# Kernel optimization log

Measured on AMD Instinct MI355X. Metric: run time of the kernel, lower is better.

The kernel has to match this reference:

```python
import jax, jax.numpy as jnp
import numpy as np

ALPHA = 0.2  # leaky relu slope
NEG_BIG = -9000000000000000.0


def setup_inputs() -> dict:
    key = jax.random.key(0)
    k1, k2, k3, k4 = jax.random.split(key, 4)
    B, N, Fin, Fout = 8, 2048, 256, 256
    h = jax.random.normal(k1, (B, N, Fin), dtype=jnp.float32)
    adj = jax.random.randint(k2, (B, N, N), 0, 2, dtype=jnp.int32)
    # xavier_uniform with gain=1.414
    gain = 1.414
    limW = gain * np.sqrt(6.0 / (Fin + Fout))
    W = jax.random.uniform(k3, (Fin, Fout), dtype=jnp.float32, minval=-limW, maxval=limW)
    lima = gain * np.sqrt(6.0 / (2 * Fout + 1))
    a = jax.random.uniform(k4, (2 * Fout, 1), dtype=jnp.float32, minval=-lima, maxval=lima)
    return {"h": h, "adj": adj, "W": W, "a": a}


def reference(h, adj, W, a):
    # Wh: [B, N, F]
    Wh = jnp.matmul(h, W)
    Fout = W.shape[1]
    a1 = a[:Fout, 0]   # scores for source node i (repeat_interleave side)
    a2 = a[Fout:, 0]   # scores for target node j (repeat side)
    # e[b,i,j] = leakyrelu(Wh[b,i]@a1 + Wh[b,j]@a2)  -- decomposed, no O(N^2 * 2F) tensor
    s1 = jnp.einsum('bnf,f->bn', Wh, a1)  # [B, N]
    s2 = jnp.einsum('bnf,f->bn', Wh, a2)  # [B, N]
    e = jax.nn.leaky_relu(s1[:, :, None] + s2[:, None, :], negative_slope=ALPHA)
    masked = jnp.where(adj > 0, e, jnp.full_like(e, NEG_BIG))
    attention = jax.nn.softmax(masked, axis=2)  # dropout=0 (eval mode)
    h_prime = jnp.matmul(attention, Wh)  # [B, N, F]
    return jax.nn.elu(h_prime)
```

## Files before the change

### kernel.cpp

```cpp
#include <hip/hip_runtime.h>

typedef __attribute__((ext_vector_type(8))) short bhalf8;
typedef __attribute__((ext_vector_type(4))) float floatx4;

#define ALPHA_LR 0.2f

__device__ __forceinline__ unsigned short f2bf(float f) {
  union { float f; unsigned int u; } v; v.f = f;
  unsigned int r = v.u + 0x7fffu + ((v.u >> 16) & 1u);
  return (unsigned short)(r >> 16);
}
__device__ __forceinline__ float bf2f(unsigned short u) {
  union { unsigned int u; float f; } v; v.u = ((unsigned int)u) << 16;
  return v.f;
}
__device__ __forceinline__ void gld16(const void* g, void* l) {
  __builtin_amdgcn_global_load_lds((const __attribute__((address_space(1))) unsigned int*)g,
                                   (__attribute__((address_space(3))) unsigned int*)l,
                                   16, 0, 0);
}

__global__ void k0w_split(const float* __restrict__ W,
                          unsigned short* __restrict__ WThi,
                          unsigned short* __restrict__ WTlo) {
  __shared__ float s[16][17];
  const int tx = threadIdx.x, ty = threadIdx.y;
  const int n0 = blockIdx.x * 16, k0 = blockIdx.y * 16;
  s[ty][tx] = W[(k0 + ty) * 256 + n0 + tx];
  __syncthreads();
  float v = s[tx][ty];
  const int k = k0 + tx, n = n0 + ty;
  unsigned short hi = f2bf(v);
  unsigned short lo = f2bf(v - bf2f(hi));
  const int idx = (k >> 5) * 8192 + n * 32 + (k & 31);
  WThi[idx] = hi;
  WTlo[idx] = lo;
}

__global__ __launch_bounds__(512, 2) void k1_mfma(const float* __restrict__ h,
                                                  const unsigned short* __restrict__ Bhi_g,
                                                  const unsigned short* __restrict__ Blo_g,
                                                  const float* __restrict__ a_g,
                                                  unsigned short* __restrict__ WhPack,
                                                  float* __restrict__ s1,
                                                  float* __restrict__ s2) {
  __shared__ unsigned short Ah[64 * 264], Al[64 * 264];
  __shared__ unsigned short Bh[2][8192], Bl[2][8192];
  __shared__ float s1red[64], s2red[64];
  const int t = threadIdx.x;
  const long r0 = (long)blockIdx.x * 64;
  const int wave = t >> 6, lane = t & 63;

  if (t < 64) { s1red[t] = 0.f; s2red[t] = 0.f; }

#pragma unroll
  for (int rep = 0; rep < 2; rep++) {
    const int off = wave * 1024 + rep * 512;
    gld16(Bhi_g + off + lane * 8, &Bh[0][off]);
    gld16(Blo_g + off + lane * 8, &Bl[0][off]);
  }

#pragma unroll
  for (int q = 0; q < 8; q++) {
    int idx = q * 512 + t;
    int row = idx >> 6, c4 = idx & 63;
    float4 x = *(const float4*)(h + (r0 + row) * 256 + c4 * 4);
    float xs[4] = {x.x, x.y, x.z, x.w};
    unsigned short hs[4], ls[4];
#pragma unroll
    for (int qq = 0; qq < 4; qq++) {
      hs[qq] = f2bf(xs[qq]);
      ls[qq] = f2bf(xs[qq] - bf2f(hs[qq]));
    }
    *(ushort4*)&Ah[row * 264 + c4 * 4] = (ushort4){hs[0], hs[1], hs[2], hs[3]};
    *(ushort4*)&Al[row * 264 + c4 * 4] = (ushort4){ls[0], ls[1], ls[2], ls[3]};
  }
  __syncthreads();

  const int wm = wave >> 2, wn = wave & 3;
  const int lhi = lane >> 4, llo = lane & 15;

  floatx4 acc[2][4];
#pragma unroll
  for (int mt = 0; mt < 2; mt++)
#pragma unroll
    for (int nt = 0; nt < 4; nt++) acc[mt][nt] = (floatx4){0.f, 0.f, 0.f, 0.f};

  for (int ks = 0; ks < 8; ks++) {
    const int cur = ks & 1, nxt = cur ^ 1, ksn = (ks + 1) & 7;
#pragma unroll
    for (int rep = 0; rep < 2; rep++) {
      const int off = wave * 1024 + rep * 512;
      gld16(Bhi_g + ksn * 8192 + off + lane * 8, &Bh[nxt][off]);
      gld16(Blo_g + ksn * 8192 + off + lane * 8, &Bl[nxt][off]);
    }

    const int k0 = ks * 32;
    bhalf8 ah[2], al[2], bh[4], bl[4];
#pragma unroll
    for (int mt = 0; mt < 2; mt++) {
      int ro = (wm * 32 + mt * 16 + llo) * 264 + k0 + lhi * 8;
      ah[mt] = *(const bhalf8*)&Ah[ro];
      al[mt] = *(const bhalf8*)&Al[ro];
    }
#pragma unroll
    for (int nt = 0; nt < 4; nt++) {
      int ro = (wn * 64 + nt * 16 + llo) * 32 + lhi * 8;
      bh[nt] = *(const bhalf8*)&Bh[cur][ro];
      bl[nt] = *(const bhalf8*)&Bl[cur][ro];
    }
#pragma unroll
    for (int mt = 0; mt < 2; mt++)
#pragma unroll
      for (int nt = 0; nt < 4; nt++) {
        acc[mt][nt] = __builtin_amdgcn_mfma_f32_16x16x32_bf16(ah[mt], bh[nt], acc[mt][nt], 0, 0, 0);
        acc[mt][nt] = __builtin_amdgcn_mfma_f32_16x16x32_bf16(ah[mt], bl[nt], acc[mt][nt], 0, 0, 0);
        acc[mt][nt] = __builtin_amdgcn_mfma_f32_16x16x32_bf16(al[mt], bh[nt], acc[mt][nt], 0, 0, 0);
      }
    __syncthreads();
  }

  float a1v[4], a2v[4];
#pragma unroll
  for (int nt = 0; nt < 4; nt++) {
    int f = wn * 64 + nt * 16 + llo;
    a1v[nt] = a_g[f];
    a2v[nt] = a_g[256 + f];
  }

  const int b = (int)(r0 >> 11);
  const int jt_base = (int)((r0 & 2047) >> 5);

#pragma unroll
  for (int mt = 0; mt < 2; mt++) {
    float p1[4], p2[4];
#pragma unroll
    for (int reg = 0; reg < 4; reg++) {
      p1[reg] = acc[mt][0][reg] * a1v[0] + acc[mt][1][reg] * a1v[1] +
                acc[mt][2][reg] * a1v[2] + acc[mt][3][reg] * a1v[3];
      p2[reg] = acc[mt][0][reg] * a2v[0] + acc[mt][1][reg] * a2v[1] +
                acc[mt][2][reg] * a2v[2] + acc[mt][3][reg] * a2v[3];
    }
#pragma unroll
    for (int off = 1; off < 16; off <<= 1) {
#pragma unroll
      for (int reg = 0; reg < 4; reg++) {
        p1[reg] += __shfl_xor(p1[reg], off);
        p2[reg] += __shfl_xor(p2[reg], off);
      }
    }
    if (llo == 0) {
#pragma unroll
      for (int reg = 0; reg < 4; reg++) {
        int il = wm * 32 + mt * 16 + lhi * 4 + reg;
        atomicAdd(&s1red[il], p1[reg]);
        atomicAdd(&s2red[il], p2[reg]);
      }
    }
#pragma unroll
    for (int nt = 0; nt < 4; nt++) {
      int f = wn * 64 + nt * 16 + llo;
      int jt = jt_base + wm;
      ushort4 pk = (ushort4){f2bf(acc[mt][nt][0]), f2bf(acc[mt][nt][1]),
                             f2bf(acc[mt][nt][2]), f2bf(acc[mt][nt][3])};
      *(ushort4*)&WhPack[((long)((b * 64 + jt) * 256 + f)) * 32 + mt * 16 + lhi * 4] = pk;
    }
  }

  __syncthreads();
  if (t < 64) {
    s1[r0 + t] = s1red[t];
    s2[r0 + t] = s2red[t];
  }
}

__global__ __launch_bounds__(256) void k2_stats(const int* __restrict__ adj,
                                                const float* __restrict__ s1,
                                                const float* __restrict__ s2,
                                                float* __restrict__ Mv,
                                                float* __restrict__ linv,
                                                unsigned int* __restrict__ packed) {
  const int t = threadIdx.x;
  const long r = blockIdx.x;
  const int b = (int)(r >> 11);
  __shared__ float red[4];
  __shared__ int redi[4];
  __shared__ unsigned char bytes[256];

  const int4* arow = (const int4*)(adj + r * 2048);
  int4 a0 = arow[t * 2], a1 = arow[t * 2 + 1];
  unsigned int m8 = (unsigned)(a0.x > 0) | ((unsigned)(a0.y > 0) << 1) |
                    ((unsigned)(a0.z > 0) << 2) | ((unsigned)(a0.w > 0) << 3) |
                    ((unsigned)(a1.x > 0) << 4) | ((unsigned)(a1.y > 0) << 5) |
                    ((unsigned)(a1.z > 0) << 6) | ((unsigned)(a1.w > 0) << 7);

  int cnt = __popc(m8);
  for (int o = 32; o; o >>= 1) cnt += __shfl_xor(cnt, o);
  if ((t & 63) == 0) redi[t >> 6] = cnt;
  __syncthreads();
  int total = redi[0] + redi[1] + redi[2] + redi[3];
  if (total == 0) m8 = 0xFFu;

  const float4* s2p = (const float4*)(s2 + (long)b * 2048);
  float4 v0 = s2p[t * 2], v1 = s2p[t * 2 + 1];
  float sv[8] = {v0.x, v0.y, v0.z, v0.w, v1.x, v1.y, v1.z, v1.w};

  float mx = -INFINITY;
#pragma unroll
  for (int q = 0; q < 8; q++)
    if ((m8 >> q) & 1) mx = fmaxf(mx, sv[q]);
  for (int o = 32; o; o >>= 1) mx = fmaxf(mx, __shfl_xor(mx, o));
  if ((t & 63) == 0) red[t >> 6] = mx;
  __syncthreads();
  mx = fmaxf(fmaxf(red[0], red[1]), fmaxf(red[2], red[3]));

  const float s1i = s1[r];
  const float xm = s1i + mx;
  const float M = fmaxf(xm, ALPHA_LR * xm);

  float lsum = 0.f;
#pragma unroll
  for (int q = 0; q < 8; q++) {
    if ((m8 >> q) & 1) {
      float x = s1i + sv[q];
      float le = fmaxf(x, ALPHA_LR * x);
      lsum += __expf(le - M);
    }
  }
  for (int o = 32; o; o >>= 1) lsum += __shfl_xor(lsum, o);
  __syncthreads();
  if ((t & 63) == 0) red[t >> 6] = lsum;
  __syncthreads();
  lsum = red[0] + red[1] + red[2] + red[3];

  if (t == 0) { Mv[r] = M; linv[r] = 1.f / lsum; }

  bytes[t] = (unsigned char)m8;
  __syncthreads();
  if (t < 64) {
    unsigned int w = (unsigned)bytes[t * 4] | ((unsigned)bytes[t * 4 + 1] << 8) |
                     ((unsigned)bytes[t * 4 + 2] << 16) | ((unsigned)bytes[t * 4 + 3] << 24);
    packed[r * 64 + t] = w;
  }
}

__global__ __launch_bounds__(512, 4) void k3_attn(const unsigned short* __restrict__ WhPack,
                                                  const unsigned int* __restrict__ packed,
                                                  const float* __restrict__ s1,
                                                  const float* __restrict__ s2,
                                                  const float* __restrict__ Mv,
                                                  const float* __restrict__ linv,
                                                  float* __restrict__ out) {
  const int t = threadIdx.x;
  const int it = blockIdx.x;
  const int b = blockIdx.y;
  const int i0 = it * 32;

  __shared__ float s2all[2048];
  __shared__ unsigned int bits[2048];
  __shared__ float s1v[32], Mvv[32], lvv[32];
  __shared__ unsigned short WhT[2][8192];
  __shared__ unsigned short P[2][1280];

  {
    const float4* src = (const float4*)(s2 + (long)b * 2048);
    ((float4*)s2all)[t] = src[t];
  }
  {
    const int4* src = (const int4*)(packed + ((long)b * 2048 + i0) * 64);
    ((int4*)bits)[t] = src[t];
  }
  if (t < 32) {
    long r = (long)b * 2048 + i0 + t;
    s1v[t] = s1[r]; Mvv[t] = Mv[r]; lvv[t] = linv[r];
  }
  __syncthreads();

  const int wave = t >> 6, lane = t & 63;
  const int wm = wave >> 2, wn = wave & 3;
  const int lhi = lane >> 4, llo = lane & 15;
  const int i_p = t >> 4;
  const int jl0 = (t & 15) * 2;

  const unsigned short* tbase = WhPack + ((long)b * 64) * 8192;

#pragma unroll
  for (int rep = 0; rep < 2; rep++) {
    const int off = wave * 1024 + rep * 512;
    gld16(tbase + off + lane * 8, &WhT[0][off]);
  }
  {
    unsigned int w = bits[i_p * 64 + 0];
    float s1i = s1v[i_p], Mi = Mvv[i_p];
    unsigned short pb[2];
#pragma unroll
    for (int q = 0; q < 2; q++) {
      int jl = jl0 + q;
      float x = s1i + s2all[jl];
      float le = fmaxf(x, ALPHA_LR * x);
      float pu = ((w >> jl) & 1u) ? __expf(le - Mi) : 0.f;
      pb[q] = f2bf(pu);
    }
    *(unsigned int*)&P[0][i_p * 40 + jl0] = (unsigned)pb[0] | ((unsigned)pb[1] << 16);
  }
  __syncthreads();

  floatx4 acc[4];
#pragma unroll
  for (int nt = 0; nt < 4; nt++) acc[nt] = (floatx4){0.f, 0.f, 0.f, 0.f};

  for (int jt = 0; jt < 64; jt++) {
    const int cur = jt & 1, nxt = cur ^ 1, jtn = (jt + 1) & 63;

#pragma unroll
    for (int rep = 0; rep < 2; rep++) {
      const int off = wave * 1024 + rep * 512;
      gld16(tbase + jtn * 8192 + off + lane * 8, &WhT[nxt][off]);
    }
    {
      unsigned int w = bits[i_p * 64 + jtn];
      float s1i = s1v[i_p], Mi = Mvv[i_p];
      unsigned short pb[2];
#pragma unroll
      for (int q = 0; q < 2; q++) {
        int jl = jl0 + q;
        float x = s1i + s2all[jtn * 32 + jl];
        float le = fmaxf(x, ALPHA_LR * x);
        float pu = ((w >> jl) & 1u) ? __expf(le - Mi) : 0.f;
        pb[q] = f2bf(pu);
      }
      *(unsigned int*)&P[nxt][i_p * 40 + jl0] = (unsigned)pb[0] | ((unsigned)pb[1] << 16);
    }
    bhalf8 af = *(const bhalf8*)&P[cur][(wm * 16 + llo) * 40 + lhi * 8];
    bhalf8 bf[4];
#pragma unroll
    for (int nt = 0; nt < 4; nt++)
      bf[nt] = *(const bhalf8*)&WhT[cur][(wn * 64 + nt * 16 + llo) * 32 + lhi * 8];
#pragma unroll
    for (int nt = 0; nt < 4; nt++)
      acc[nt] = __builtin_amdgcn_mfma_f32_16x16x32_bf16(af, bf[nt], acc[nt], 0, 0, 0);
    __syncthreads();
  }

#pragma unroll
  for (int nt = 0; nt < 4; nt++) {
#pragma unroll
    for (int reg = 0; reg < 4; reg++) {
      int il = wm * 16 + lhi * 4 + reg;
      int f = wn * 64 + nt * 16 + llo;
      float v = acc[nt][reg] * lvv[il];
      v = v > 0.f ? v : expm1f(v);
      out[((long)(b * 2048 + i0 + il)) * 256 + f] = v;
    }
  }
}

extern "C" void kernel_launch(void* const* d_in, const int* in_sizes, int n_in,
                              void* d_out, int out_size, void* d_ws, size_t ws_size,
                              hipStream_t stream) {
  const float* h = (const float*)d_in[0];
  const int* adj = (const int*)d_in[1];
  const float* W = (const float*)d_in[2];
  const float* a = (const float*)d_in[3];
  float* out = (float*)d_out;

  char* ws = (char*)d_ws;
  unsigned short* WhPack = (unsigned short*)ws;
  unsigned int* packed = (unsigned int*)(ws + 8388608);
  unsigned short* WThi = (unsigned short*)(ws + 12582912);
  unsigned short* WTlo = (unsigned short*)(ws + 12713984);
  float* s1 = (float*)(ws + 12845056);
  float* s2 = (float*)(ws + 12910592);
  float* Mv = (float*)(ws + 12976128);
  float* linv = (float*)(ws + 13041664);

  hipLaunchKernelGGL(k0w_split, dim3(16, 16), dim3(16, 16), 0, stream, W, WThi, WTlo);
  hipLaunchKernelGGL(k1_mfma, dim3(256), dim3(512), 0, stream, h, WThi, WTlo, a,
                     WhPack, s1, s2);
  hipLaunchKernelGGL(k2_stats, dim3(16384), dim3(256), 0, stream, adj, s1, s2, Mv, linv, packed);
  hipLaunchKernelGGL(k3_attn, dim3(64, 8), dim3(512), 0, stream, WhPack, packed, s1, s2, Mv, linv, out);
}
```

Baseline: 265.4 us.

## Retile attention kernel: 128-row by 64-feature blocks, P in registers, B from global

The attention-times-Wh kernel now tiles 128 rows by 64 output features per 256-thread block, replacing 32 rows by all 256 features. Each wave computes its P fragments directly in registers from the mask bits and s1/s2, so the shared-memory P buffer and the per-step __syncthreads go away. Wh fragments are loaded straight from global into registers with a two-deep software prefetch, where before they were staged into LDS via global_load_lds. The grid grows to 512 blocks, and the exp work is now repeated across the four feature-chunk blocks, which adds redundant transcendental computation.

```diff
diff --git a/kernel.cpp b/kernel.cpp
--- a/kernel.cpp
+++ b/kernel.cpp
@@ -244,113 +244,121 @@
   }
 }
 
-__global__ __launch_bounds__(512, 4) void k3_attn(const unsigned short* __restrict__ WhPack,
+__global__ __launch_bounds__(256, 3) void k3_attn(const unsigned short* __restrict__ WhPack,
                                                   const unsigned int* __restrict__ packed,
-                                                  const float* __restrict__ s1,
-                                                  const float* __restrict__ s2,
-                                                  const float* __restrict__ Mv,
-                                                  const float* __restrict__ linv,
+                                                  const float* __restrict__ s1g,
+                                                  const float* __restrict__ s2g,
+                                                  const float* __restrict__ Mg,
+                                                  const float* __restrict__ lg,
                                                   float* __restrict__ out) {
   const int t = threadIdx.x;
-  const int it = blockIdx.x;
-  const int b = blockIdx.y;
-  const int i0 = it * 32;
+  const int fc = blockIdx.x;
+  const int ry = blockIdx.y;
+  const int b = blockIdx.z;
+  const int rowbase = ry * 128;
 
   __shared__ float s2all[2048];
-  __shared__ unsigned int bits[2048];
-  __shared__ float s1v[32], Mvv[32], lvv[32];
-  __shared__ unsigned short WhT[2][8192];
-  __shared__ unsigned short P[2][1280];
+  __shared__ unsigned int bits[128 * 68];
+  __shared__ float lvv[128];
 
   {
-    const float4* src = (const float4*)(s2 + (long)b * 2048);
-    ((float4*)s2all)[t] = src[t];
+    const float4* src = (const float4*)(s2g + (long)b * 2048);
+    float4* dst = (float4*)s2all;
+    dst[t] = src[t];
+    dst[256 + t] = src[256 + t];
   }
   {
-    const int4* src = (const int4*)(packed + ((long)b * 2048 + i0) * 64);
-    ((int4*)bits)[t] = src[t];
-  }
-  if (t < 32) {
-    long r = (long)b * 2048 + i0 + t;
-    s1v[t] = s1[r]; Mvv[t] = Mv[r]; lvv[t] = linv[r];
-  }
-  __syncthreads();
+    const int4* src = (const int4*)(packed + ((long)b * 2048 + rowbase) * 64);
+#pragma unroll
+    for (int q = 0; q < 8; q++) {
+      int idx = q * 256 + t;
+      int row = idx >> 4, c = idx & 15;
+      int4 v = src[idx];
+      *(int4*)&bits[row * 68 + c * 4] = v;
+    }
+  }
+  if (t < 128) lvv[t] = lg[(long)b * 2048 + rowbase + t];
 
   const int wave = t >> 6, lane = t & 63;
-  const int wm = wave >> 2, wn = wave & 3;
   const int lhi = lane >> 4, llo = lane & 15;
-  const int i_p = t >> 4;
-  const int jl0 = (t & 15) * 2;
-
-  const unsigned short* tbase = WhPack + ((long)b * 64) * 8192;
-
-#pragma unroll
-  for (int rep = 0; rep < 2; rep++) {
-    const int off = wave * 1024 + rep * 512;
-    gld16(tbase + off + lane * 8, &WhT[0][off]);
-  }
-  {
-    unsigned int w = bits[i_p * 64 + 0];
-    float s1i = s1v[i_p], Mi = Mvv[i_p];
-    unsigned short pb[2];
-#pragma unroll
-    for (int q = 0; q < 2; q++) {
-      int jl = jl0 + q;
-      float x = s1i + s2all[jl];
-      float le = fmaxf(x, ALPHA_LR * x);
-      float pu = ((w >> jl) & 1u) ? __expf(le - Mi) : 0.f;
-      pb[q] = f2bf(pu);
-    }
-    *(unsigned int*)&P[0][i_p * 40 + jl0] = (unsigned)pb[0] | ((unsigned)pb[1] << 16);
-  }
-  __syncthreads();
-
-  floatx4 acc[4];
-#pragma unroll
-  for (int nt = 0; nt < 4; nt++) acc[nt] = (floatx4){0.f, 0.f, 0.f, 0.f};
-
-  for (int jt = 0; jt < 64; jt++) {
-    const int cur = jt & 1, nxt = cur ^ 1, jtn = (jt + 1) & 63;
-
-#pragma unroll
-    for (int rep = 0; rep < 2; rep++) {
-      const int off = wave * 1024 + rep * 512;
-      gld16(tbase + jtn * 8192 + off + lane * 8, &WhT[nxt][off]);
-    }
-    {
-      unsigned int w = bits[i_p * 64 + jtn];
-      float s1i = s1v[i_p], Mi = Mvv[i_p];
-      unsigned short pb[2];
-#pragma unroll
-      for (int q = 0; q < 2; q++) {
-        int jl = jl0 + q;
-        float x = s1i + s2all[jtn * 32 + jl];
-        float le = fmaxf(x, ALPHA_LR * x);
-        float pu = ((w >> jl) & 1u) ? __expf(le - Mi) : 0.f;
-        pb[q] = f2bf(pu);
+  const int wrow = wave * 32;
+
+  float s1i[2], Mi[2];
+#pragma unroll
+  for (int mt = 0; mt < 2; mt++) {
+    long r = (long)b * 2048 + rowbase + wrow + mt * 16 + llo;
+    s1i[mt] = s1g[r];
+    Mi[mt] = Mg[r];
+  }
+  __syncthreads();
+
+  const unsigned short* Bl = WhPack + (long)b * 64 * 8192 + fc * 64 * 32 + llo * 32 + lhi * 8;
+
+  floatx4 acc[2][4];
+#pragma unroll
+  for (int mt = 0; mt < 2; mt++)
+#pragma unroll
+    for (int nt = 0; nt < 4; nt++) acc[mt][nt] = (floatx4){0.f, 0.f, 0.f, 0.f};
+
+  bhalf8 B0[4], B1[4];
+#pragma unroll
+  for (int nt = 0; nt < 4; nt++) B0[nt] = *(const bhalf8*)(Bl + nt * 512);
+
+#define K3_STEP(JT, BUF)                                                        \
+  {                                                                             \
+    const int jt_ = (JT);                                                       \
+    float4 s2lo = *(const float4*)&s2all[jt_ * 32 + lhi * 8];                   \
+    float4 s2hi = *(const float4*)&s2all[jt_ * 32 + lhi * 8 + 4];               \
+    float s2v[8] = {s2lo.x, s2lo.y, s2lo.z, s2lo.w,                             \
+                    s2hi.x, s2hi.y, s2hi.z, s2hi.w};                            \
+    bhalf8 afr[2];                                                              \
+    _Pragma("unroll") for (int mt = 0; mt < 2; mt++) {                          \
+      unsigned int wv = bits[(wrow + mt * 16 + llo) * 68 + jt_];                \
+      union { unsigned int u[4]; bhalf8 v; } au;                                \
+      _Pragma("unroll") for (int pp = 0; pp < 4; pp++) {                        \
+        float x0 = ((wv >> (lhi * 8 + 2 * pp)) & 1u) ? (s1i[mt] + s2v[2 * pp])  \
+                                                     : -1e30f;                  \
+        float x1 = ((wv >> (lhi * 8 + 2 * pp + 1)) & 1u)                        \
+                       ? (s1i[mt] + s2v[2 * pp + 1]) : -1e30f;                  \
+        x0 = fmaxf(x0, ALPHA_LR * x0);                                          \
+        x1 = fmaxf(x1, ALPHA_LR * x1);                                          \
+        union { float f; unsigned int u; } u0, u1;                              \
+        u0.f = __expf(x0 - Mi[mt]);                                             \
+        u1.f = __expf(x1 - Mi[mt]);                                             \
+        au.u[pp] = (u0.u >> 16) | (u1.u & 0xffff0000u);                         \
+      }                                                                         \
+      afr[mt] = au.v;                                                           \
+    }                                                                           \
+    _Pragma("unroll") for (int mt = 0; mt < 2; mt++)                            \
+        _Pragma("unroll") for (int nt = 0; nt < 4; nt++)                        \
+            acc[mt][nt] = __builtin_amdgcn_mfma_f32_16x16x32_bf16(              \
+                afr[mt], BUF[nt], acc[mt][nt], 0, 0, 0);                        \
+  }
+
+  for (int jt = 0; jt < 64; jt += 2) {
+    const unsigned short* p1 = Bl + (jt + 1) * 8192;
+#pragma unroll
+    for (int nt = 0; nt < 4; nt++) B1[nt] = *(const bhalf8*)(p1 + nt * 512);
+    K3_STEP(jt, B0)
+    const int jn = (jt + 2 < 64) ? jt + 2 : 63;
+    const unsigned short* p0 = Bl + jn * 8192;
+#pragma unroll
+    for (int nt = 0; nt < 4; nt++) B0[nt] = *(const bhalf8*)(p0 + nt * 512);
+    K3_STEP(jt + 1, B1)
+  }
+#undef K3_STEP
+
+#pragma unroll
+  for (int mt = 0; mt < 2; mt++) {
+#pragma unroll
+    for (int nt = 0; nt < 4; nt++) {
+#pragma unroll
+      for (int reg = 0; reg < 4; reg++) {
+        int brow = wrow + mt * 16 + lhi * 4 + reg;
+        float v = acc[mt][nt][reg] * lvv[brow];
+        v = v > 0.f ? v : expm1f(v);
+        out[((long)b * 2048 + rowbase + brow) * 256 + fc * 64 + nt * 16 + llo] = v;
       }
-      *(unsigned int*)&P[nxt][i_p * 40 + jl0] = (unsigned)pb[0] | ((unsigned)pb[1] << 16);
-    }
-    bhalf8 af = *(const bhalf8*)&P[cur][(wm * 16 + llo) * 40 + lhi * 8];
-    bhalf8 bf[4];
-#pragma unroll
-    for (int nt = 0; nt < 4; nt++)
-      bf[nt] = *(const bhalf8*)&WhT[cur][(wn * 64 + nt * 16 + llo) * 32 + lhi * 8];
-#pragma unroll
-    for (int nt = 0; nt < 4; nt++)
-      acc[nt] = __builtin_amdgcn_mfma_f32_16x16x32_bf16(af, bf[nt], acc[nt], 0, 0, 0);
-    __syncthreads();
-  }
-
-#pragma unroll
-  for (int nt = 0; nt < 4; nt++) {
-#pragma unroll
-    for (int reg = 0; reg < 4; reg++) {
-      int il = wm * 16 + lhi * 4 + reg;
-      int f = wn * 64 + nt * 16 + llo;
-      float v = acc[nt][reg] * lvv[il];
-      v = v > 0.f ? v : expm1f(v);
-      out[((long)(b * 2048 + i0 + il)) * 256 + f] = v;
     }
   }
 }
@@ -378,5 +386,6 @@
   hipLaunchKernelGGL(k1_mfma, dim3(256), dim3(512), 0, stream, h, WThi, WTlo, a,
                      WhPack, s1, s2);
   hipLaunchKernelGGL(k2_stats, dim3(16384), dim3(256), 0, stream, adj, s1, s2, Mv, linv, packed);
-  hipLaunchKernelGGL(k3_attn, dim3(64, 8), dim3(512), 0, stream, WhPack, packed, s1, s2, Mv, linv, out);
-}
+  hipLaunchKernelGGL(k3_attn, dim3(4, 16, 8), dim3(256), 0, stream, WhPack, packed,
+                     s1, s2, Mv, linv, out);
+}
```

Measured after the change: 270.5 us. About the same (+1.9%).

## Fuse adjacency masking and softmax statistics into attention kernel, drop stats pass

Applied to the files above, without the earlier changes.

Removes the separate statistics kernel that read the int32 adjacency matrix, packed it into bitmasks and computed per-row max and normalizer. The attention kernel now reads adjacency directly, prefetching one tile ahead, and accumulates the softmax denominator on the fly. It uses a per-batch global max of s2, computed with an atomic max in the projection kernel, as a stabilizing upper bound. This saves one full pass over adjacency, the packed-mask round trip and a kernel launch. In exchange, the shift is looser than the masked row max, so exponentials could underflow more. The denominator is summed in fp32 while the matmul uses bf16 probabilities, and fully masked rows now give zero instead of a uniform average.

```diff
diff --git a/kernel.cpp b/kernel.cpp
--- a/kernel.cpp
+++ b/kernel.cpp
@@ -22,9 +22,11 @@
 
 __global__ void k0w_split(const float* __restrict__ W,
                           unsigned short* __restrict__ WThi,
-                          unsigned short* __restrict__ WTlo) {
+                          unsigned short* __restrict__ WTlo,
+                          unsigned int* __restrict__ s2maxEnc) {
   __shared__ float s[16][17];
   const int tx = threadIdx.x, ty = threadIdx.y;
+  if (blockIdx.x == 0 && blockIdx.y == 0 && ty == 0 && tx < 8) s2maxEnc[tx] = 0u;
   const int n0 = blockIdx.x * 16, k0 = blockIdx.y * 16;
   s[ty][tx] = W[(k0 + ty) * 256 + n0 + tx];
   __syncthreads();
@@ -43,7 +45,8 @@
                                                   const float* __restrict__ a_g,
                                                   unsigned short* __restrict__ WhPack,
                                                   float* __restrict__ s1,
-                                                  float* __restrict__ s2) {
+                                                  float* __restrict__ s2,
+                                                  unsigned int* __restrict__ s2maxEnc) {
   __shared__ unsigned short Ah[64 * 264], Al[64 * 264];
   __shared__ unsigned short Bh[2][8192], Bl[2][8192];
   __shared__ float s1red[64], s2red[64];
@@ -171,110 +174,34 @@
   if (t < 64) {
     s1[r0 + t] = s1red[t];
     s2[r0 + t] = s2red[t];
-  }
-}
-
-__global__ __launch_bounds__(256) void k2_stats(const int* __restrict__ adj,
-                                                const float* __restrict__ s1,
-                                                const float* __restrict__ s2,
-                                                float* __restrict__ Mv,
-                                                float* __restrict__ linv,
-                                                unsigned int* __restrict__ packed) {
-  const int t = threadIdx.x;
-  const long r = blockIdx.x;
-  const int b = (int)(r >> 11);
-  __shared__ float red[4];
-  __shared__ int redi[4];
-  __shared__ unsigned char bytes[256];
-
-  const int4* arow = (const int4*)(adj + r * 2048);
-  int4 a0 = arow[t * 2], a1 = arow[t * 2 + 1];
-  unsigned int m8 = (unsigned)(a0.x > 0) | ((unsigned)(a0.y > 0) << 1) |
-                    ((unsigned)(a0.z > 0) << 2) | ((unsigned)(a0.w > 0) << 3) |
-                    ((unsigned)(a1.x > 0) << 4) | ((unsigned)(a1.y > 0) << 5) |
-                    ((unsigned)(a1.z > 0) << 6) | ((unsigned)(a1.w > 0) << 7);
-
-  int cnt = __popc(m8);
-  for (int o = 32; o; o >>= 1) cnt += __shfl_xor(cnt, o);
-  if ((t & 63) == 0) redi[t >> 6] = cnt;
-  __syncthreads();
-  int total = redi[0] + redi[1] + redi[2] + redi[3];
-  if (total == 0) m8 = 0xFFu;
-
-  const float4* s2p = (const float4*)(s2 + (long)b * 2048);
-  float4 v0 = s2p[t * 2], v1 = s2p[t * 2 + 1];
-  float sv[8] = {v0.x, v0.y, v0.z, v0.w, v1.x, v1.y, v1.z, v1.w};
-
-  float mx = -INFINITY;
-#pragma unroll
-  for (int q = 0; q < 8; q++)
-    if ((m8 >> q) & 1) mx = fmaxf(mx, sv[q]);
-  for (int o = 32; o; o >>= 1) mx = fmaxf(mx, __shfl_xor(mx, o));
-  if ((t & 63) == 0) red[t >> 6] = mx;
-  __syncthreads();
-  mx = fmaxf(fmaxf(red[0], red[1]), fmaxf(red[2], red[3]));
-
-  const float s1i = s1[r];
-  const float xm = s1i + mx;
-  const float M = fmaxf(xm, ALPHA_LR * xm);
-
-  float lsum = 0.f;
-#pragma unroll
-  for (int q = 0; q < 8; q++) {
-    if ((m8 >> q) & 1) {
-      float x = s1i + sv[q];
-      float le = fmaxf(x, ALPHA_LR * x);
-      lsum += __expf(le - M);
-    }
-  }
-  for (int o = 32; o; o >>= 1) lsum += __shfl_xor(lsum, o);
-  __syncthreads();
-  if ((t & 63) == 0) red[t >> 6] = lsum;
-  __syncthreads();
-  lsum = red[0] + red[1] + red[2] + red[3];
-
-  if (t == 0) { Mv[r] = M; linv[r] = 1.f / lsum; }
-
-  bytes[t] = (unsigned char)m8;
-  __syncthreads();
-  if (t < 64) {
-    unsigned int w = (unsigned)bytes[t * 4] | ((unsigned)bytes[t * 4 + 1] << 8) |
-                     ((unsigned)bytes[t * 4 + 2] << 16) | ((unsigned)bytes[t * 4 + 3] << 24);
-    packed[r * 64 + t] = w;
+    float v = s2red[t];
+#pragma unroll
+    for (int o = 32; o; o >>= 1) v = fmaxf(v, __shfl_xor(v, o));
+    if (t == 0) {
+      unsigned int u = __float_as_uint(v);
+      unsigned int key = (u & 0x80000000u) ? ~u : (u | 0x80000000u);
+      atomicMax(s2maxEnc + b, key);
+    }
   }
 }
 
 __global__ __launch_bounds__(512, 4) void k3_attn(const unsigned short* __restrict__ WhPack,
-                                                  const unsigned int* __restrict__ packed,
-                                                  const float* __restrict__ s1,
-                                                  const float* __restrict__ s2,
-                                                  const float* __restrict__ Mv,
-                                                  const float* __restrict__ linv,
+                                                  const int* __restrict__ adj,
+                                                  const float* __restrict__ s1g,
+                                                  const float* __restrict__ s2g,
+                                                  const unsigned int* __restrict__ s2maxEnc,
                                                   float* __restrict__ out) {
   const int t = threadIdx.x;
-  const int it = blockIdx.x;
+  const int i0 = blockIdx.x * 32;
   const int b = blockIdx.y;
-  const int i0 = it * 32;
+  const long gr0 = (long)b * 2048 + i0;
 
   __shared__ float s2all[2048];
-  __shared__ unsigned int bits[2048];
-  __shared__ float s1v[32], Mvv[32], lvv[32];
   __shared__ unsigned short WhT[2][8192];
   __shared__ unsigned short P[2][1280];
-
-  {
-    const float4* src = (const float4*)(s2 + (long)b * 2048);
-    ((float4*)s2all)[t] = src[t];
-  }
-  {
-    const int4* src = (const int4*)(packed + ((long)b * 2048 + i0) * 64);
-    ((int4*)bits)[t] = src[t];
-  }
-  if (t < 32) {
-    long r = (long)b * 2048 + i0 + t;
-    s1v[t] = s1[r]; Mvv[t] = Mv[r]; lvv[t] = linv[r];
-  }
-  __syncthreads();
+  __shared__ float lvv[32];
+
+  ((float4*)s2all)[t] = ((const float4*)(s2g + (long)b * 2048))[t];
 
   const int wave = t >> 6, lane = t & 63;
   const int wm = wave >> 2, wn = wave & 3;
@@ -282,6 +209,14 @@
   const int i_p = t >> 4;
   const int jl0 = (t & 15) * 2;
 
+  const float s1i = s1g[gr0 + i_p];
+  const unsigned int ek = s2maxEnc[b];
+  const float s2max = (ek & 0x80000000u) ? __uint_as_float(ek & 0x7fffffffu)
+                                         : __uint_as_float(~ek);
+  const float xm = s1i + s2max;
+  const float Mi = fmaxf(xm, ALPHA_LR * xm);
+
+  const int* aptr = adj + (gr0 + i_p) * 2048 + jl0;
   const unsigned short* tbase = WhPack + ((long)b * 64) * 8192;
 
 #pragma unroll
@@ -289,19 +224,22 @@
     const int off = wave * 1024 + rep * 512;
     gld16(tbase + off + lane * 8, &WhT[0][off]);
   }
+  int2 aj0 = *(const int2*)aptr;
+  int2 aj1 = *(const int2*)(aptr + 32);
+
+  __syncthreads();
+
+  float lsum;
   {
-    unsigned int w = bits[i_p * 64 + 0];
-    float s1i = s1v[i_p], Mi = Mvv[i_p];
-    unsigned short pb[2];
-#pragma unroll
-    for (int q = 0; q < 2; q++) {
-      int jl = jl0 + q;
-      float x = s1i + s2all[jl];
-      float le = fmaxf(x, ALPHA_LR * x);
-      float pu = ((w >> jl) & 1u) ? __expf(le - Mi) : 0.f;
-      pb[q] = f2bf(pu);
-    }
-    *(unsigned int*)&P[0][i_p * 40 + jl0] = (unsigned)pb[0] | ((unsigned)pb[1] << 16);
+    float x0 = s1i + s2all[jl0];
+    float x1 = s1i + s2all[jl0 + 1];
+    x0 = fmaxf(x0, ALPHA_LR * x0);
+    x1 = fmaxf(x1, ALPHA_LR * x1);
+    float e0 = (aj0.x > 0) ? __expf(x0 - Mi) : 0.f;
+    float e1 = (aj0.y > 0) ? __expf(x1 - Mi) : 0.f;
+    lsum = e0 + e1;
+    *(unsigned int*)&P[0][i_p * 40 + jl0] =
+        (unsigned)f2bf(e0) | ((unsigned)f2bf(e1) << 16);
   }
   __syncthreads();
 
@@ -310,26 +248,26 @@
   for (int nt = 0; nt < 4; nt++) acc[nt] = (floatx4){0.f, 0.f, 0.f, 0.f};
 
   for (int jt = 0; jt < 64; jt++) {
-    const int cur = jt & 1, nxt = cur ^ 1, jtn = (jt + 1) & 63;
-
-#pragma unroll
-    for (int rep = 0; rep < 2; rep++) {
-      const int off = wave * 1024 + rep * 512;
-      gld16(tbase + jtn * 8192 + off + lane * 8, &WhT[nxt][off]);
-    }
-    {
-      unsigned int w = bits[i_p * 64 + jtn];
-      float s1i = s1v[i_p], Mi = Mvv[i_p];
-      unsigned short pb[2];
-#pragma unroll
-      for (int q = 0; q < 2; q++) {
-        int jl = jl0 + q;
-        float x = s1i + s2all[jtn * 32 + jl];
-        float le = fmaxf(x, ALPHA_LR * x);
-        float pu = ((w >> jl) & 1u) ? __expf(le - Mi) : 0.f;
-        pb[q] = f2bf(pu);
+    const int cur = jt & 1, nxt = cur ^ 1;
+    if (jt < 63) {
+      const int jtn = jt + 1;
+#pragma unroll
+      for (int rep = 0; rep < 2; rep++) {
+        const int off = wave * 1024 + rep * 512;
+        gld16(tbase + jtn * 8192 + off + lane * 8, &WhT[nxt][off]);
       }
-      *(unsigned int*)&P[nxt][i_p * 40 + jl0] = (unsigned)pb[0] | ((unsigned)pb[1] << 16);
+      const int2 ajc = aj1;
+      const int jpf = (jt + 2 < 64) ? jt + 2 : 63;
+      aj1 = *(const int2*)(aptr + jpf * 32);
+      float x0 = s1i + s2all[jtn * 32 + jl0];
+      float x1 = s1i + s2all[jtn * 32 + jl0 + 1];
+      x0 = fmaxf(x0, ALPHA_LR * x0);
+      x1 = fmaxf(x1, ALPHA_LR * x1);
+      float e0 = (ajc.x > 0) ? __expf(x0 - Mi) : 0.f;
+      float e1 = (ajc.y > 0) ? __expf(x1 - Mi) : 0.f;
+      lsum += e0 + e1;
+      *(unsigned int*)&P[nxt][i_p * 40 + jl0] =
+          (unsigned)f2bf(e0) | ((unsigned)f2bf(e1) << 16);
     }
     bhalf8 af = *(const bhalf8*)&P[cur][(wm * 16 + llo) * 40 + lhi * 8];
     bhalf8 bf[4];
@@ -341,6 +279,13 @@
       acc[nt] = __builtin_amdgcn_mfma_f32_16x16x32_bf16(af, bf[nt], acc[nt], 0, 0, 0);
     __syncthreads();
   }
+
+  lsum += __shfl_xor(lsum, 1);
+  lsum += __shfl_xor(lsum, 2);
+  lsum += __shfl_xor(lsum, 4);
+  lsum += __shfl_xor(lsum, 8);
+  if ((t & 15) == 0) lvv[i_p] = 1.f / fmaxf(lsum, 1e-35f);
+  __syncthreads();
 
 #pragma unroll
   for (int nt = 0; nt < 4; nt++) {
@@ -350,7 +295,7 @@
       int f = wn * 64 + nt * 16 + llo;
       float v = acc[nt][reg] * lvv[il];
       v = v > 0.f ? v : expm1f(v);
-      out[((long)(b * 2048 + i0 + il)) * 256 + f] = v;
+      out[(gr0 + il) * 256 + f] = v;
     }
   }
 }
@@ -366,17 +311,15 @@
 
   char* ws = (char*)d_ws;
   unsigned short* WhPack = (unsigned short*)ws;
-  unsigned int* packed = (unsigned int*)(ws + 8388608);
-  unsigned short* WThi = (unsigned short*)(ws + 12582912);
-  unsigned short* WTlo = (unsigned short*)(ws + 12713984);
-  float* s1 = (float*)(ws + 12845056);
-  float* s2 = (float*)(ws + 12910592);
-  float* Mv = (float*)(ws + 12976128);
-  float* linv = (float*)(ws + 13041664);
-
-  hipLaunchKernelGGL(k0w_split, dim3(16, 16), dim3(16, 16), 0, stream, W, WThi, WTlo);
+  unsigned short* WThi = (unsigned short*)(ws + 8388608);
+  unsigned short* WTlo = (unsigned short*)(ws + 8519680);
+  float* s1 = (float*)(ws + 8650752);
+  float* s2 = (float*)(ws + 8716288);
+  unsigned int* s2maxEnc = (unsigned int*)(ws + 8781824);
+
+  hipLaunchKernelGGL(k0w_split, dim3(16, 16), dim3(16, 16), 0, stream, W, WThi, WTlo, s2maxEnc);
   hipLaunchKernelGGL(k1_mfma, dim3(256), dim3(512), 0, stream, h, WThi, WTlo, a,
-                     WhPack, s1, s2);
-  hipLaunchKernelGGL(k2_stats, dim3(16384), dim3(256), 0, stream, adj, s1, s2, Mv, linv, packed);
-  hipLaunchKernelGGL(k3_attn, dim3(64, 8), dim3(512), 0, stream, WhPack, packed, s1, s2, Mv, linv, out);
-}
+                     WhPack, s1, s2, s2maxEnc);
+  hipLaunchKernelGGL(k3_attn, dim3(64, 8), dim3(512), 0, stream, WhPack, adj,
+                     s1, s2, s2maxEnc, out);
+}
```

Measured after the change: 253.4 us. 1.05x faster.
